# Kernel tuning notes

Hardware: AMD Instinct MI355X
Metric: run time of the kernel (lower is better)

The kernel has to match this reference:

```python
import math
import jax, jax.numpy as jnp
import numpy as np

HIDDEN = 1024

def setup_inputs() -> dict:
    key = jax.random.key(0)
    kx, kq, kk, kv = jax.random.split(key, 4)
    scale = 1.0 / math.sqrt(HIDDEN)
    x = jax.random.normal(kx, (4, 2048, HIDDEN), dtype=jnp.float32)
    # nn.Linear weights, stored as [out, in] like torch; y = x @ W.T
    Wq = jax.random.normal(kq, (HIDDEN, HIDDEN), dtype=jnp.float32) * scale
    Wk = jax.random.normal(kk, (HIDDEN, HIDDEN), dtype=jnp.float32) * scale
    Wv = jax.random.normal(kv, (HIDDEN, HIDDEN), dtype=jnp.float32) * scale
    return {"x": x, "Wq": Wq, "Wk": Wk, "Wv": Wv}

def reference(x, Wq, Wk, Wv):
    # Q,K,V: [b, s, d]
    Q = jnp.einsum('bsd,ed->bse', x, Wq)
    K = jnp.einsum('bsd,ed->bse', x, Wk)
    V = jnp.einsum('bsd,ed->bse', x, Wv)
    scores = jnp.einsum('bqd,bkd->bqk', Q, K) / math.sqrt(x.shape[-1])
    att = jax.nn.softmax(scores, axis=-1)  # stable max-subtracted softmax, same math as _softmax
    return jnp.einsum('bqk,bkd->bqd', att, V)
```

## Files before the change

### kernel.cpp

```cpp
#include <hip/hip_runtime.h>
#include <stdint.h>

typedef unsigned int uint;
typedef unsigned short ushort;
typedef __attribute__((ext_vector_type(8))) short short8;
typedef __attribute__((ext_vector_type(16))) float floatx16;

#define MEG (1024u * 1024u)

__device__ inline ushort f2b(float f) {
  union { float f; uint u; } c; c.f = f;
  uint u = c.u;
  u = (u + 0x7fffu + ((u >> 16) & 1u)) >> 16;
  return (ushort)u;
}
__device__ inline float b2f(ushort u) {
  union { uint i; float f; } c; c.i = ((uint)u) << 16; return c.f;
}

__device__ inline void gl_lds16(const ushort* g, ushort* l) {
  __builtin_amdgcn_global_load_lds(
      (const __attribute__((address_space(1))) void*)g,
      (__attribute__((address_space(3))) void*)l, 16, 0, 0);
}

__global__ __launch_bounds__(256) void cvt_all(
    const float* __restrict__ x,  const float* __restrict__ wq,
    const float* __restrict__ wk, const float* __restrict__ wv,
    ushort* __restrict__ xb, ushort* __restrict__ wb,
    float* __restrict__ ls)
{
  const int b = blockIdx.x;
  if (b >= 5632) {
    float4 z = make_float4(0.f, 0.f, 0.f, 0.f);
#pragma unroll
    for (int j = 0; j < 8; ++j)
      ((float4*)ls)[threadIdx.x * 8 + j] = z;
    return;
  }
  const float* s; ushort* d; int i;
  if (b < 4096) {
    s = x; d = xb; i = b * 256 + threadIdx.x;
  } else {
    int t = b - 4096;
    int wsel = t >> 9;
    s = (wsel == 0) ? wq : (wsel == 1) ? wk : wv;
    d = wb + (size_t)wsel * MEG;
    i = (t & 511) * 256 + threadIdx.x;
  }
  float4 a = ((const float4*)s)[i * 2];
  float4 c = ((const float4*)s)[i * 2 + 1];
  short8 v;
  v[0] = (short)f2b(a.x); v[1] = (short)f2b(a.y);
  v[2] = (short)f2b(a.z); v[3] = (short)f2b(a.w);
  v[4] = (short)f2b(c.x); v[5] = (short)f2b(c.y);
  v[6] = (short)f2b(c.z); v[7] = (short)f2b(c.w);
  ((short8*)d)[i] = v;
}

template <int MODE, int BN>
__device__ __forceinline__ void gemm_core(
    const ushort* __restrict__ A, int lda, size_t sA,
    const ushort* __restrict__ B, int ldb, size_t sB,
    void* __restrict__ C, int ldc, size_t sC,
    int K, float scale, float* __restrict__ Lsum)
{
  constexpr int NJ = BN / 64;
  constexpr int NB = BN / 32;
  __shared__ ushort As[128 * 64];
  __shared__ ushort Bs[BN * 64];

  const int tid = threadIdx.x;
  const int bz  = blockIdx.z;
  A += (size_t)bz * sA;
  B += (size_t)bz * sB;

  const int m0 = blockIdx.y * 128;
  const int n0 = blockIdx.x * BN;

  const int lane = tid & 63;
  const int w    = tid >> 6;
  const int l32  = lane & 31;
  const int lh   = lane >> 5;
  const int mw   = w >> 1;
  const int nw   = w & 1;

  const int srow = tid >> 3;
  const ushort* agp[4];
  const ushort* bgp[NB];
#pragma unroll
  for (int c4 = 0; c4 < 4; ++c4) {
    int r   = c4 * 32 + srow;
    int col = (((tid & 7) ^ ((r ^ (r >> 3)) & 7))) * 8;
    agp[c4] = A + (size_t)(m0 + r) * lda + col;
  }
#pragma unroll
  for (int cb = 0; cb < NB; ++cb) {
    int r   = cb * 32 + srow;
    int col = (((tid & 7) ^ ((r ^ (r >> 3)) & 7))) * 8;
    bgp[cb] = B + (size_t)(n0 + r) * ldb + col;
  }

  int arow[2], aswz[2], brow[NJ], bswz[NJ];
#pragma unroll
  for (int t = 0; t < 2; ++t) {
    arow[t] = mw * 64 + t * 32 + l32;
    aswz[t] = (arow[t] ^ (arow[t] >> 3)) & 7;
  }
#pragma unroll
  for (int t = 0; t < NJ; ++t) {
    brow[t] = nw * (BN / 2) + t * 32 + l32;
    bswz[t] = (brow[t] ^ (brow[t] >> 3)) & 7;
  }

  floatx16 acc[2][NJ];
#pragma unroll
  for (int i = 0; i < 2; ++i)
#pragma unroll
    for (int j = 0; j < NJ; ++j)
#pragma unroll
      for (int r = 0; r < 16; ++r) acc[i][j][r] = 0.f;

  for (int k0 = 0; k0 < K; k0 += 64) {
    __syncthreads();
#pragma unroll
    for (int c4 = 0; c4 < 4; ++c4) {
      gl_lds16(agp[c4], &As[(c4 * 32 + w * 8) * 64]);
      agp[c4] += 64;
    }
#pragma unroll
    for (int cb = 0; cb < NB; ++cb) {
      gl_lds16(bgp[cb], &Bs[(cb * 32 + w * 8) * 64]);
      bgp[cb] += 64;
    }
    __syncthreads();

#pragma unroll
    for (int s = 0; s < 4; ++s) {
      short8 af[2], bf[NJ];
#pragma unroll
      for (int t = 0; t < 2; ++t)
        af[t] = *(const short8*)&As[arow[t] * 64 + (((s * 2 + lh) ^ aswz[t]) * 8)];
#pragma unroll
      for (int t = 0; t < NJ; ++t)
        bf[t] = *(const short8*)&Bs[brow[t] * 64 + (((s * 2 + lh) ^ bswz[t]) * 8)];
#pragma unroll
      for (int i = 0; i < 2; ++i)
#pragma unroll
        for (int j = 0; j < NJ; ++j)
          acc[i][j] = __builtin_amdgcn_mfma_f32_32x32x16_bf16(
              af[i], bf[j], acc[i][j], 0, 0, 0);
    }
  }

  if constexpr (MODE == 0) {
#pragma unroll
    for (int i = 0; i < 2; ++i)
#pragma unroll
      for (int j = 0; j < NJ; ++j) {
        const int mbase = m0 + mw * 64 + i * 32 + 4 * lh;
        const int ng    = n0 + nw * (BN / 2) + j * 32 + l32;
        if (ng < 2048) {
          ushort* dst = (ushort*)C + (size_t)(ng >> 10) * (8u * MEG);
          const int nn = ng & 1023;
#pragma unroll
          for (int g = 0; g < 4; ++g)
#pragma unroll
            for (int r = 0; r < 4; ++r)
              dst[(size_t)(mbase + 8 * g + r) * 1024 + nn] =
                  f2b(acc[i][j][4 * g + r]);
        } else {
          ushort* Vo = (ushort*)C + (size_t)16 * MEG;
#pragma unroll
          for (int g = 0; g < 4; ++g) {
            uint lo = (uint)f2b(acc[i][j][4 * g + 0]) |
                      ((uint)f2b(acc[i][j][4 * g + 1]) << 16);
            uint hi = (uint)f2b(acc[i][j][4 * g + 2]) |
                      ((uint)f2b(acc[i][j][4 * g + 3]) << 16);
            *(uint2*)&Vo[(size_t)(ng - 2048) * 8192 + mbase + 8 * g] =
                make_uint2(lo, hi);
          }
        }
      }
  } else if constexpr (MODE == 1) {
    ushort* Cb = (ushort*)C + (size_t)bz * sC;
    float* Lb = Lsum + (size_t)bz * 2048;
    const int ng0 = n0 + nw * (BN / 2) + l32;
#pragma unroll
    for (int i = 0; i < 2; ++i) {
      const int mbase = m0 + mw * 64 + i * 32 + 4 * lh;
#pragma unroll
      for (int g = 0; g < 4; ++g)
#pragma unroll
        for (int r = 0; r < 4; ++r) {
          const int mg = mbase + 8 * g + r;
          float p0 = exp2f(acc[i][0][4 * g + r] * scale);
          float p1 = exp2f(acc[i][NJ - 1][4 * g + r] * scale);
          ushort u0 = f2b(p0), u1 = f2b(p1);
          Cb[(size_t)mg * ldc + ng0]      = u0;
          Cb[(size_t)mg * ldc + ng0 + 32] = u1;
          float ps = b2f(u0) + b2f(u1);
#pragma unroll
          for (int d = 1; d < 32; d <<= 1) ps += __shfl_xor(ps, d);
          if (l32 == 0) atomicAdd(&Lb[mg], ps);
        }
    }
  } else {
    float* Cb = (float*)C + (size_t)bz * sC;
    const float* Lb = Lsum + (size_t)bz * 2048;
#pragma unroll
    for (int i = 0; i < 2; ++i) {
      const int mbase = m0 + mw * 64 + i * 32 + 4 * lh;
#pragma unroll
      for (int g = 0; g < 4; ++g)
#pragma unroll
        for (int r = 0; r < 4; ++r) {
          const int mg = mbase + 8 * g + r;
          const float inv = 1.0f / Lb[mg];
#pragma unroll
          for (int j = 0; j < NJ; ++j) {
            const int ng = n0 + nw * (BN / 2) + j * 32 + l32;
            Cb[(size_t)mg * ldc + ng] = acc[i][j][4 * g + r] * inv;
          }
        }
    }
  }
}

__global__ __launch_bounds__(256, 3) void gemm_qkv(
    const ushort* __restrict__ A, int lda, size_t sA,
    const ushort* __restrict__ B, int ldb, size_t sB,
    void* __restrict__ C, int ldc, size_t sC, int K, float scale,
    float* __restrict__ Lsum) {
  gemm_core<0, 128>(A, lda, sA, B, ldb, sB, C, ldc, sC, K, scale, Lsum);
}
__global__ __launch_bounds__(256, 4) void gemm_s(
    const ushort* __restrict__ A, int lda, size_t sA,
    const ushort* __restrict__ B, int ldb, size_t sB,
    void* __restrict__ C, int ldc, size_t sC, int K, float scale,
    float* __restrict__ Lsum) {
  gemm_core<1, 128>(A, lda, sA, B, ldb, sB, C, ldc, sC, K, scale, Lsum);
}
__global__ __launch_bounds__(256, 3) void gemm_pv(
    const ushort* __restrict__ A, int lda, size_t sA,
    const ushort* __restrict__ B, int ldb, size_t sB,
    void* __restrict__ C, int ldc, size_t sC, int K, float scale,
    float* __restrict__ Lsum) {
  gemm_core<2, 128>(A, lda, sA, B, ldb, sB, C, ldc, sC, K, scale, Lsum);
}

extern "C" void kernel_launch(void* const* d_in, const int* in_sizes, int n_in,
                              void* d_out, int out_size, void* d_ws, size_t ws_size,
                              hipStream_t stream) {
  const float* x  = (const float*)d_in[0];
  const float* Wq = (const float*)d_in[1];
  const float* Wk = (const float*)d_in[2];
  const float* Wv = (const float*)d_in[3];
  float* outp = (float*)d_out;

  const float SCALE = 1.4426950408889634f / 32.0f;

  ushort* W0 = (ushort*)d_ws;
  ushort* Qb = W0;
  ushort* Kb = W0 + (size_t)8 * MEG;
  ushort* Vt = W0 + (size_t)16 * MEG;
  ushort* xb = W0 + (size_t)24 * MEG;
  ushort* Wb = W0 + (size_t)32 * MEG;
  ushort* Pb = W0 + (size_t)24 * MEG;

  const size_t NEED_FULL = ((size_t)40 * MEG) * 2 + 4 * 2048 * 4;
  const bool full = ws_size >= NEED_FULL;
  float* Ls = full ? (float*)(W0 + (size_t)40 * MEG)
                   : (float*)(W0 + (size_t)28 * MEG);

  cvt_all<<<5633, 256, 0, stream>>>(x, Wq, Wk, Wv, xb, Wb, Ls);

  gemm_qkv<<<dim3(24, 64, 1), 256, 0, stream>>>(
      xb, 1024, 0, Wb, 1024, 0, Qb, 1024, 0, 1024, 1.f, nullptr);

  if (full) {
    gemm_s<<<dim3(16, 16, 4), 256, 0, stream>>>(
        Qb, 1024, (size_t)2048 * 1024, Kb, 1024, (size_t)2048 * 1024,
        Pb, 2048, (size_t)2048 * 2048, 1024, SCALE, Ls);
    gemm_pv<<<dim3(8, 16, 4), 256, 0, stream>>>(
        Pb, 2048, (size_t)2048 * 2048, Vt, 8192, 2048,
        outp, 1024, (size_t)2048 * 1024, 2048, 1.f, Ls);
  } else {
    for (int b = 0; b < 4; ++b) {
      (void)hipMemsetAsync(Ls, 0, 2048 * sizeof(float), stream);
      gemm_s<<<dim3(16, 16, 1), 256, 0, stream>>>(
          Qb + (size_t)b * 2048 * 1024, 1024, 0,
          Kb + (size_t)b * 2048 * 1024, 1024, 0,
          Pb, 2048, 0, 1024, SCALE, Ls);
      gemm_pv<<<dim3(8, 16, 1), 256, 0, stream>>>(
          Pb, 2048, 0, Vt + (size_t)b * 2048, 8192, 0,
          outp + (size_t)b * 2048 * 1024, 1024, 0, 2048, 1.f, Ls);
    }
  }
}
```

Before: 249.1 us.

## Move GEMMs to 256-row tiles with 8 waves and a 4-stage async LDS pipeline

The shared bf16 GEMM core moves from 128xBN tiles with BK=64 and single-buffered loads to 256x256 (or 256x128) tiles with BK=32, run by 512-thread blocks. A four-slot LDS ring is filled with global_load_lds prefetches three tiles ahead. Explicit vmcnt/lgkmcnt waits, raw barriers and s_setprio around the MFMA bursts are meant to overlap global loads with matrix math and raise arithmetic intensity per block. The cost is a larger LDS footprint (about 128KB for BN=256, which limits blocks per CU), fewer blocks in the grid, and more complex hand-managed synchronisation.

Measured after the change: 265.7 us. 6.7% more time.

```diff
diff --git a/kernel.cpp b/kernel.cpp
--- a/kernel.cpp
+++ b/kernel.cpp
@@ -22,6 +22,19 @@
   __builtin_amdgcn_global_load_lds(
       (const __attribute__((address_space(1))) void*)g,
       (__attribute__((address_space(3))) void*)l, 16, 0, 0);
+}
+
+__device__ __forceinline__ void bar() {
+  asm volatile("" ::: "memory");
+  __builtin_amdgcn_s_barrier();
+  asm volatile("" ::: "memory");
+}
+template <int N>
+__device__ __forceinline__ void vm_wait() {
+  asm volatile("s_waitcnt vmcnt(%0)" :: "n"(N) : "memory");
+}
+__device__ __forceinline__ void lgkm0() {
+  asm volatile("s_waitcnt lgkmcnt(0)" ::: "memory");
 }
 
 __global__ __launch_bounds__(256) void cvt_all(
@@ -65,101 +78,177 @@
     void* __restrict__ C, int ldc, size_t sC,
     int K, float scale, float* __restrict__ Lsum)
 {
-  constexpr int NJ = BN / 64;
-  constexpr int NB = BN / 32;
-  __shared__ ushort As[128 * 64];
-  __shared__ ushort Bs[BN * 64];
+  static_assert(BN == 256 || BN == 128, "BN");
+  constexpr int BM = 256;
+  constexpr int BK = 32;
+  constexpr int WAVES_M = (BN == 256) ? 2 : 4;
+  constexpr int WAVES_N = 8 / WAVES_M;
+  constexpr int MI = BM / (WAVES_M * 32);
+  constexpr int NJ = BN / (WAVES_N * 32);
+  constexpr int A_ISS = BM / 128;
+  constexpr int B_ISS = BN / 128;
+  constexpr int LPT = A_ISS + B_ISS;
+
+  __shared__ ushort As[4 * BM * BK];
+  __shared__ ushort Bs[4 * BN * BK];
 
   const int tid = threadIdx.x;
   const int bz  = blockIdx.z;
   A += (size_t)bz * sA;
   B += (size_t)bz * sB;
 
-  const int m0 = blockIdx.y * 128;
+  const int m0 = blockIdx.y * BM;
   const int n0 = blockIdx.x * BN;
 
   const int lane = tid & 63;
   const int w    = tid >> 6;
   const int l32  = lane & 31;
   const int lh   = lane >> 5;
-  const int mw   = w >> 1;
-  const int nw   = w & 1;
-
-  const int srow = tid >> 3;
-  const ushort* agp[4];
-  const ushort* bgp[NB];
-#pragma unroll
-  for (int c4 = 0; c4 < 4; ++c4) {
-    int r   = c4 * 32 + srow;
-    int col = (((tid & 7) ^ ((r ^ (r >> 3)) & 7))) * 8;
-    agp[c4] = A + (size_t)(m0 + r) * lda + col;
-  }
-#pragma unroll
-  for (int cb = 0; cb < NB; ++cb) {
-    int r   = cb * 32 + srow;
-    int col = (((tid & 7) ^ ((r ^ (r >> 3)) & 7))) * 8;
-    bgp[cb] = B + (size_t)(n0 + r) * ldb + col;
-  }
-
-  int arow[2], aswz[2], brow[NJ], bswz[NJ];
-#pragma unroll
-  for (int t = 0; t < 2; ++t) {
-    arow[t] = mw * 64 + t * 32 + l32;
-    aswz[t] = (arow[t] ^ (arow[t] >> 3)) & 7;
-  }
-#pragma unroll
-  for (int t = 0; t < NJ; ++t) {
-    brow[t] = nw * (BN / 2) + t * 32 + l32;
-    bswz[t] = (brow[t] ^ (brow[t] >> 3)) & 7;
-  }
-
-  floatx16 acc[2][NJ];
-#pragma unroll
-  for (int i = 0; i < 2; ++i)
+  const int mw   = (BN == 256) ? (w >> 2) : (w >> 1);
+  const int nw   = (BN == 256) ? (w & 3) : (w & 1);
+
+  const int srow = tid >> 2;
+  const int sch  = tid & 3;
+  const ushort* agp[A_ISS];
+  const ushort* bgp[B_ISS];
+#pragma unroll
+  for (int q = 0; q < A_ISS; ++q) {
+    int r = q * 128 + srow;
+    agp[q] = A + (size_t)(m0 + r) * lda + ((sch ^ ((r ^ (r >> 3)) & 3)) * 8);
+  }
+#pragma unroll
+  for (int q = 0; q < B_ISS; ++q) {
+    int r = q * 128 + srow;
+    bgp[q] = B + (size_t)(n0 + r) * ldb + ((sch ^ ((r ^ (r >> 3)) & 3)) * 8);
+  }
+
+  int oa[MI], sa[MI], ob[NJ], sb[NJ];
+#pragma unroll
+  for (int i = 0; i < MI; ++i) {
+    int r = mw * (MI * 32) + i * 32 + l32;
+    oa[i] = r * BK; sa[i] = (r ^ (r >> 3)) & 3;
+  }
+#pragma unroll
+  for (int j = 0; j < NJ; ++j) {
+    int r = nw * (NJ * 32) + j * 32 + l32;
+    ob[j] = r * BK; sb[j] = (r ^ (r >> 3)) & 3;
+  }
+
+  floatx16 acc[MI][NJ];
+#pragma unroll
+  for (int i = 0; i < MI; ++i)
 #pragma unroll
     for (int j = 0; j < NJ; ++j)
 #pragma unroll
       for (int r = 0; r < 16; ++r) acc[i][j][r] = 0.f;
 
-  for (int k0 = 0; k0 < K; k0 += 64) {
-    __syncthreads();
-#pragma unroll
-    for (int c4 = 0; c4 < 4; ++c4) {
-      gl_lds16(agp[c4], &As[(c4 * 32 + w * 8) * 64]);
-      agp[c4] += 64;
-    }
-#pragma unroll
-    for (int cb = 0; cb < NB; ++cb) {
-      gl_lds16(bgp[cb], &Bs[(cb * 32 + w * 8) * 64]);
-      bgp[cb] += 64;
-    }
-    __syncthreads();
-
-#pragma unroll
-    for (int s = 0; s < 4; ++s) {
-      short8 af[2], bf[NJ];
-#pragma unroll
-      for (int t = 0; t < 2; ++t)
-        af[t] = *(const short8*)&As[arow[t] * 64 + (((s * 2 + lh) ^ aswz[t]) * 8)];
-#pragma unroll
-      for (int t = 0; t < NJ; ++t)
-        bf[t] = *(const short8*)&Bs[brow[t] * 64 + (((s * 2 + lh) ^ bswz[t]) * 8)];
+  const int nt = K / BK;
+
+#pragma unroll
+  for (int pt = 0; pt < 3; ++pt) {
+    ushort* Ad = &As[pt * (BM * BK)];
+    ushort* Bd = &Bs[pt * (BN * BK)];
+#pragma unroll
+    for (int q = 0; q < A_ISS; ++q) {
+      gl_lds16(agp[q], Ad + (q * 128 + w * 16) * BK); agp[q] += BK;
+    }
+#pragma unroll
+    for (int q = 0; q < B_ISS; ++q) {
+      gl_lds16(bgp[q], Bd + (q * 128 + w * 16) * BK); bgp[q] += BK;
+    }
+  }
+  vm_wait<2 * LPT>();
+  bar();
+
+  for (int t = 0; t < nt; ++t) {
+    const ushort* At = &As[(t & 3) * (BM * BK)];
+    const ushort* Bt = &Bs[(t & 3) * (BN * BK)];
+    ushort* Ad = &As[((t + 3) & 3) * (BM * BK)];
+    ushort* Bd = &Bs[((t + 3) & 3) * (BN * BK)];
+    const bool st = (t + 3 < nt);
+
+    short8 bf[NJ][2];
+#pragma unroll
+    for (int j = 0; j < NJ; ++j)
+#pragma unroll
+      for (int ks = 0; ks < 2; ++ks)
+        bf[j][ks] = *(const short8*)(Bt + ob[j] + ((((ks * 2) + lh) ^ sb[j]) << 3));
+
+    short8 af[2][2];
+#pragma unroll
+    for (int i = 0; i < 2; ++i)
+#pragma unroll
+      for (int ks = 0; ks < 2; ++ks)
+        af[i][ks] = *(const short8*)(At + oa[i] + ((((ks * 2) + lh) ^ sa[i]) << 3));
+    if (st) {
+#pragma unroll
+      for (int q = 0; q < A_ISS; ++q) {
+        gl_lds16(agp[q], Ad + (q * 128 + w * 16) * BK); agp[q] += BK;
+      }
+      if constexpr (BN == 128) {
+#pragma unroll
+        for (int q = 0; q < B_ISS; ++q) {
+          gl_lds16(bgp[q], Bd + (q * 128 + w * 16) * BK); bgp[q] += BK;
+        }
+      }
+    }
+    bar();
+    lgkm0();
+    __builtin_amdgcn_s_setprio(1);
+#pragma unroll
+    for (int i = 0; i < 2; ++i)
+#pragma unroll
+      for (int j = 0; j < NJ; ++j)
+#pragma unroll
+        for (int ks = 0; ks < 2; ++ks)
+          acc[i][j] = __builtin_amdgcn_mfma_f32_32x32x16_bf16(
+              af[i][ks], bf[j][ks], acc[i][j], 0, 0, 0);
+    __builtin_amdgcn_s_setprio(0);
+    if constexpr (BN == 128) {
+      if (t + 3 < nt)      vm_wait<2 * LPT>();
+      else if (t + 2 < nt) vm_wait<LPT>();
+      else                 vm_wait<0>();
+    }
+    bar();
+
+    if constexpr (BN == 256) {
 #pragma unroll
       for (int i = 0; i < 2; ++i)
 #pragma unroll
+        for (int ks = 0; ks < 2; ++ks)
+          af[i][ks] = *(const short8*)(At + oa[2 + i] + ((((ks * 2) + lh) ^ sa[2 + i]) << 3));
+      if (st) {
+#pragma unroll
+        for (int q = 0; q < B_ISS; ++q) {
+          gl_lds16(bgp[q], Bd + (q * 128 + w * 16) * BK); bgp[q] += BK;
+        }
+      }
+      bar();
+      lgkm0();
+      __builtin_amdgcn_s_setprio(1);
+#pragma unroll
+      for (int i = 0; i < 2; ++i)
+#pragma unroll
         for (int j = 0; j < NJ; ++j)
-          acc[i][j] = __builtin_amdgcn_mfma_f32_32x32x16_bf16(
-              af[i], bf[j], acc[i][j], 0, 0, 0);
+#pragma unroll
+          for (int ks = 0; ks < 2; ++ks)
+            acc[2 + i][j] = __builtin_amdgcn_mfma_f32_32x32x16_bf16(
+                af[i][ks], bf[j][ks], acc[2 + i][j], 0, 0, 0);
+      __builtin_amdgcn_s_setprio(0);
+      if (t + 3 < nt)      vm_wait<2 * LPT>();
+      else if (t + 2 < nt) vm_wait<LPT>();
+      else                 vm_wait<0>();
+      bar();
     }
   }
 
   if constexpr (MODE == 0) {
 #pragma unroll
-    for (int i = 0; i < 2; ++i)
+    for (int i = 0; i < MI; ++i)
 #pragma unroll
       for (int j = 0; j < NJ; ++j) {
-        const int mbase = m0 + mw * 64 + i * 32 + 4 * lh;
-        const int ng    = n0 + nw * (BN / 2) + j * 32 + l32;
+        const int mbase = m0 + mw * (MI * 32) + i * 32 + 4 * lh;
+        const int ng    = n0 + nw * (NJ * 32) + j * 32 + l32;
         if (ng < 2048) {
           ushort* dst = (ushort*)C + (size_t)(ng >> 10) * (8u * MEG);
           const int nn = ng & 1023;
@@ -185,10 +274,10 @@
   } else if constexpr (MODE == 1) {
     ushort* Cb = (ushort*)C + (size_t)bz * sC;
     float* Lb = Lsum + (size_t)bz * 2048;
-    const int ng0 = n0 + nw * (BN / 2) + l32;
-#pragma unroll
-    for (int i = 0; i < 2; ++i) {
-      const int mbase = m0 + mw * 64 + i * 32 + 4 * lh;
+    const int ng0 = n0 + nw * (NJ * 32) + l32;
+#pragma unroll
+    for (int i = 0; i < MI; ++i) {
+      const int mbase = m0 + mw * (MI * 32) + i * 32 + 4 * lh;
 #pragma unroll
       for (int g = 0; g < 4; ++g)
 #pragma unroll
@@ -209,8 +298,8 @@
     float* Cb = (float*)C + (size_t)bz * sC;
     const float* Lb = Lsum + (size_t)bz * 2048;
 #pragma unroll
-    for (int i = 0; i < 2; ++i) {
-      const int mbase = m0 + mw * 64 + i * 32 + 4 * lh;
+    for (int i = 0; i < MI; ++i) {
+      const int mbase = m0 + mw * (MI * 32) + i * 32 + 4 * lh;
 #pragma unroll
       for (int g = 0; g < 4; ++g)
 #pragma unroll
@@ -219,7 +308,7 @@
           const float inv = 1.0f / Lb[mg];
 #pragma unroll
           for (int j = 0; j < NJ; ++j) {
-            const int ng = n0 + nw * (BN / 2) + j * 32 + l32;
+            const int ng = n0 + nw * (NJ * 32) + j * 32 + l32;
             Cb[(size_t)mg * ldc + ng] = acc[i][j][4 * g + r] * inv;
           }
         }
@@ -227,21 +316,21 @@
   }
 }
 
-__global__ __launch_bounds__(256, 3) void gemm_qkv(
+__global__ __launch_bounds__(512, 2) void gemm_qkv(
     const ushort* __restrict__ A, int lda, size_t sA,
     const ushort* __restrict__ B, int ldb, size_t sB,
     void* __restrict__ C, int ldc, size_t sC, int K, float scale,
     float* __restrict__ Lsum) {
-  gemm_core<0, 128>(A, lda, sA, B, ldb, sB, C, ldc, sC, K, scale, Lsum);
-}
-__global__ __launch_bounds__(256, 4) void gemm_s(
+  gemm_core<0, 256>(A, lda, sA, B, ldb, sB, C, ldc, sC, K, scale, Lsum);
+}
+__global__ __launch_bounds__(512, 2) void gemm_s(
     const ushort* __restrict__ A, int lda, size_t sA,
     const ushort* __restrict__ B, int ldb, size_t sB,
     void* __restrict__ C, int ldc, size_t sC, int K, float scale,
     float* __restrict__ Lsum) {
-  gemm_core<1, 128>(A, lda, sA, B, ldb, sB, C, ldc, sC, K, scale, Lsum);
-}
-__global__ __launch_bounds__(256, 3) void gemm_pv(
+  gemm_core<1, 256>(A, lda, sA, B, ldb, sB, C, ldc, sC, K, scale, Lsum);
+}
+__global__ __launch_bounds__(512, 2) void gemm_pv(
     const ushort* __restrict__ A, int lda, size_t sA,
     const ushort* __restrict__ B, int ldb, size_t sB,
     void* __restrict__ C, int ldc, size_t sC, int K, float scale,
@@ -275,24 +364,24 @@
 
   cvt_all<<<5633, 256, 0, stream>>>(x, Wq, Wk, Wv, xb, Wb, Ls);
 
-  gemm_qkv<<<dim3(24, 64, 1), 256, 0, stream>>>(
+  gemm_qkv<<<dim3(12, 32, 1), 512, 0, stream>>>(
       xb, 1024, 0, Wb, 1024, 0, Qb, 1024, 0, 1024, 1.f, nullptr);
 
   if (full) {
-    gemm_s<<<dim3(16, 16, 4), 256, 0, stream>>>(
+    gemm_s<<<dim3(8, 8, 4), 512, 0, stream>>>(
         Qb, 1024, (size_t)2048 * 1024, Kb, 1024, (size_t)2048 * 1024,
         Pb, 2048, (size_t)2048 * 2048, 1024, SCALE, Ls);
-    gemm_pv<<<dim3(8, 16, 4), 256, 0, stream>>>(
+    gemm_pv<<<dim3(8, 8, 4), 512, 0, stream>>>(
         Pb, 2048, (size_t)2048 * 2048, Vt, 8192, 2048,
         outp, 1024, (size_t)2048 * 1024, 2048, 1.f, Ls);
   } else {
     for (int b = 0; b < 4; ++b) {
       (void)hipMemsetAsync(Ls, 0, 2048 * sizeof(float), stream);
-      gemm_s<<<dim3(16, 16, 1), 256, 0, stream>>>(
+      gemm_s<<<dim3(8, 8, 1), 512, 0, stream>>>(
           Qb + (size_t)b * 2048 * 1024, 1024, 0,
           Kb + (size_t)b * 2048 * 1024, 1024, 0,
           Pb, 2048, 0, 1024, SCALE, Ls);
-      gemm_pv<<<dim3(8, 16, 1), 256, 0, stream>>>(
+      gemm_pv<<<dim3(8, 8, 1), 512, 0, stream>>>(
           Pb, 2048, 0, Vt + (size_t)b * 2048, 8192, 0,
           outp + (size_t)b * 2048 * 1024, 1024, 0, 2048, 1.f, Ls);
     }
```

## Use 256-wide tiles with double-buffered LDS pipeline across all three GEMMs

Applied to the files above, without the earlier changes.

Each block now computes a 256xBN tile (BN 256 for the QKV and score GEMMs, 128 for the PV GEMM) with 512 threads and larger per-wave fragments. The LDS staging is double-buffered, so the next K-slice's global-to-LDS loads are issued while the current slice is consumed, and there is one barrier per iteration instead of two. Fragment reads are software-pipelined against the MFMAs, and s_setprio is raised around the matrix ops. The goal is more reuse per loaded byte and hiding load latency behind compute. The cost is 128KB of LDS per block, which allows only one block per CU, and far fewer blocks per grid (about one wave for the attention GEMMs), which can leave CUs idle or unbalanced.

Result: slower. 262.8 us (+5.5%).

```diff
diff --git a/kernel.cpp b/kernel.cpp
--- a/kernel.cpp
+++ b/kernel.cpp
@@ -65,101 +65,138 @@
     void* __restrict__ C, int ldc, size_t sC,
     int K, float scale, float* __restrict__ Lsum)
 {
-  constexpr int NJ = BN / 64;
-  constexpr int NB = BN / 32;
-  __shared__ ushort As[128 * 64];
-  __shared__ ushort Bs[BN * 64];
+  static_assert(BN == 256 || BN == 128, "BN");
+  constexpr int BM = 256;
+  constexpr int BK = 64;
+  constexpr int WM = (BN == 256) ? 2 : 4;
+  constexpr int MI = BM / (WM * 32);
+  constexpr int NJ = BN / ((8 / WM) * 32);
+  constexpr int AI = BM / 64;
+  constexpr int BI = BN / 64;
+  constexpr int ASLOT = BM * BK;
+  constexpr int BSLOT = BN * BK;
+
+  __shared__ __align__(16) ushort As[2 * ASLOT];
+  __shared__ __align__(16) ushort Bs[2 * BSLOT];
 
   const int tid = threadIdx.x;
   const int bz  = blockIdx.z;
   A += (size_t)bz * sA;
   B += (size_t)bz * sB;
 
-  const int m0 = blockIdx.y * 128;
+  const int m0 = blockIdx.y * BM;
   const int n0 = blockIdx.x * BN;
 
   const int lane = tid & 63;
   const int w    = tid >> 6;
   const int l32  = lane & 31;
   const int lh   = lane >> 5;
-  const int mw   = w >> 1;
-  const int nw   = w & 1;
+  const int mw   = (BN == 256) ? (w >> 2) : (w >> 1);
+  const int nw   = (BN == 256) ? (w & 3) : (w & 1);
 
   const int srow = tid >> 3;
-  const ushort* agp[4];
-  const ushort* bgp[NB];
-#pragma unroll
-  for (int c4 = 0; c4 < 4; ++c4) {
-    int r   = c4 * 32 + srow;
-    int col = (((tid & 7) ^ ((r ^ (r >> 3)) & 7))) * 8;
-    agp[c4] = A + (size_t)(m0 + r) * lda + col;
-  }
-#pragma unroll
-  for (int cb = 0; cb < NB; ++cb) {
-    int r   = cb * 32 + srow;
-    int col = (((tid & 7) ^ ((r ^ (r >> 3)) & 7))) * 8;
-    bgp[cb] = B + (size_t)(n0 + r) * ldb + col;
-  }
-
-  int arow[2], aswz[2], brow[NJ], bswz[NJ];
-#pragma unroll
-  for (int t = 0; t < 2; ++t) {
-    arow[t] = mw * 64 + t * 32 + l32;
-    aswz[t] = (arow[t] ^ (arow[t] >> 3)) & 7;
-  }
-#pragma unroll
-  for (int t = 0; t < NJ; ++t) {
-    brow[t] = nw * (BN / 2) + t * 32 + l32;
-    bswz[t] = (brow[t] ^ (brow[t] >> 3)) & 7;
-  }
-
-  floatx16 acc[2][NJ];
-#pragma unroll
-  for (int i = 0; i < 2; ++i)
+  const int sch  = tid & 7;
+  const ushort* agp[AI];
+  const ushort* bgp[BI];
+#pragma unroll
+  for (int q = 0; q < AI; ++q) {
+    int r = q * 64 + srow;
+    agp[q] = A + (size_t)(m0 + r) * lda + ((sch ^ ((r ^ (r >> 3)) & 7)) * 8);
+  }
+#pragma unroll
+  for (int q = 0; q < BI; ++q) {
+    int r = q * 64 + srow;
+    bgp[q] = B + (size_t)(n0 + r) * ldb + ((sch ^ ((r ^ (r >> 3)) & 7)) * 8);
+  }
+
+  int oa[MI], sa[MI], ob[NJ], sb[NJ];
+#pragma unroll
+  for (int i = 0; i < MI; ++i) {
+    int r = mw * (MI * 32) + i * 32 + l32;
+    oa[i] = r * BK; sa[i] = (r ^ (r >> 3)) & 7;
+  }
+#pragma unroll
+  for (int j = 0; j < NJ; ++j) {
+    int r = nw * (NJ * 32) + j * 32 + l32;
+    ob[j] = r * BK; sb[j] = (r ^ (r >> 3)) & 7;
+  }
+
+  floatx16 acc[MI][NJ];
+#pragma unroll
+  for (int i = 0; i < MI; ++i)
 #pragma unroll
     for (int j = 0; j < NJ; ++j)
 #pragma unroll
       for (int r = 0; r < 16; ++r) acc[i][j][r] = 0.f;
 
-  for (int k0 = 0; k0 < K; k0 += 64) {
+  const int nt = K / BK;
+
+#define STAGE(slot)                                                     \
+  {                                                                     \
+    ushort* Ad = &As[(slot) * ASLOT];                                   \
+    ushort* Bd = &Bs[(slot) * BSLOT];                                   \
+    _Pragma("unroll")                                                   \
+    for (int q = 0; q < AI; ++q) {                                      \
+      gl_lds16(agp[q], Ad + (q * 64 + w * 8) * BK); agp[q] += BK;       \
+    }                                                                   \
+    _Pragma("unroll")                                                   \
+    for (int q = 0; q < BI; ++q) {                                      \
+      gl_lds16(bgp[q], Bd + (q * 64 + w * 8) * BK); bgp[q] += BK;       \
+    }                                                                   \
+  }
+
+  STAGE(0);
+  __syncthreads();
+
+  for (int t = 0; t < nt; ++t) {
+    const ushort* At = &As[(t & 1) * ASLOT];
+    const ushort* Bt = &Bs[(t & 1) * BSLOT];
+    if (t + 1 < nt) STAGE((t + 1) & 1);
+
+    short8 af[2][MI], bf[2][NJ];
+
+#define RD(ks, buf)                                                         \
+    {                                                                       \
+      _Pragma("unroll")                                                     \
+      for (int i = 0; i < MI; ++i)                                          \
+        af[buf][i] = *(const short8*)&At[oa[i] + ((((ks)*2 + lh) ^ sa[i]) << 3)]; \
+      _Pragma("unroll")                                                     \
+      for (int j = 0; j < NJ; ++j)                                          \
+        bf[buf][j] = *(const short8*)&Bt[ob[j] + ((((ks)*2 + lh) ^ sb[j]) << 3)]; \
+    }
+#define MM(buf)                                                         \
+    {                                                                   \
+      __builtin_amdgcn_s_setprio(1);                                    \
+      _Pragma("unroll")                                                 \
+      for (int i = 0; i < MI; ++i)                                      \
+        _Pragma("unroll")                                               \
+        for (int j = 0; j < NJ; ++j)                                    \
+          acc[i][j] = __builtin_amdgcn_mfma_f32_32x32x16_bf16(          \
+              af[buf][i], bf[buf][j], acc[i][j], 0, 0, 0);              \
+      __builtin_amdgcn_s_setprio(0);                                    \
+    }
+
+    RD(0, 0);
+    RD(1, 1);
+    MM(0);
+    RD(2, 0);
+    MM(1);
+    RD(3, 1);
+    MM(0);
+    MM(1);
     __syncthreads();
-#pragma unroll
-    for (int c4 = 0; c4 < 4; ++c4) {
-      gl_lds16(agp[c4], &As[(c4 * 32 + w * 8) * 64]);
-      agp[c4] += 64;
-    }
-#pragma unroll
-    for (int cb = 0; cb < NB; ++cb) {
-      gl_lds16(bgp[cb], &Bs[(cb * 32 + w * 8) * 64]);
-      bgp[cb] += 64;
-    }
-    __syncthreads();
-
-#pragma unroll
-    for (int s = 0; s < 4; ++s) {
-      short8 af[2], bf[NJ];
-#pragma unroll
-      for (int t = 0; t < 2; ++t)
-        af[t] = *(const short8*)&As[arow[t] * 64 + (((s * 2 + lh) ^ aswz[t]) * 8)];
-#pragma unroll
-      for (int t = 0; t < NJ; ++t)
-        bf[t] = *(const short8*)&Bs[brow[t] * 64 + (((s * 2 + lh) ^ bswz[t]) * 8)];
-#pragma unroll
-      for (int i = 0; i < 2; ++i)
-#pragma unroll
-        for (int j = 0; j < NJ; ++j)
-          acc[i][j] = __builtin_amdgcn_mfma_f32_32x32x16_bf16(
-              af[i], bf[j], acc[i][j], 0, 0, 0);
-    }
-  }
+#undef RD
+#undef MM
+  }
+#undef STAGE
 
   if constexpr (MODE == 0) {
 #pragma unroll
-    for (int i = 0; i < 2; ++i)
+    for (int i = 0; i < MI; ++i)
 #pragma unroll
       for (int j = 0; j < NJ; ++j) {
-        const int mbase = m0 + mw * 64 + i * 32 + 4 * lh;
-        const int ng    = n0 + nw * (BN / 2) + j * 32 + l32;
+        const int mbase = m0 + mw * (MI * 32) + i * 32 + 4 * lh;
+        const int ng    = n0 + nw * (NJ * 32) + j * 32 + l32;
         if (ng < 2048) {
           ushort* dst = (ushort*)C + (size_t)(ng >> 10) * (8u * MEG);
           const int nn = ng & 1023;
@@ -185,10 +222,10 @@
   } else if constexpr (MODE == 1) {
     ushort* Cb = (ushort*)C + (size_t)bz * sC;
     float* Lb = Lsum + (size_t)bz * 2048;
-    const int ng0 = n0 + nw * (BN / 2) + l32;
-#pragma unroll
-    for (int i = 0; i < 2; ++i) {
-      const int mbase = m0 + mw * 64 + i * 32 + 4 * lh;
+    const int ng0 = n0 + nw * (NJ * 32) + l32;
+#pragma unroll
+    for (int i = 0; i < MI; ++i) {
+      const int mbase = m0 + mw * (MI * 32) + i * 32 + 4 * lh;
 #pragma unroll
       for (int g = 0; g < 4; ++g)
 #pragma unroll
@@ -209,8 +246,8 @@
     float* Cb = (float*)C + (size_t)bz * sC;
     const float* Lb = Lsum + (size_t)bz * 2048;
 #pragma unroll
-    for (int i = 0; i < 2; ++i) {
-      const int mbase = m0 + mw * 64 + i * 32 + 4 * lh;
+    for (int i = 0; i < MI; ++i) {
+      const int mbase = m0 + mw * (MI * 32) + i * 32 + 4 * lh;
 #pragma unroll
       for (int g = 0; g < 4; ++g)
 #pragma unroll
@@ -219,7 +256,7 @@
           const float inv = 1.0f / Lb[mg];
 #pragma unroll
           for (int j = 0; j < NJ; ++j) {
-            const int ng = n0 + nw * (BN / 2) + j * 32 + l32;
+            const int ng = n0 + nw * (NJ * 32) + j * 32 + l32;
             Cb[(size_t)mg * ldc + ng] = acc[i][j][4 * g + r] * inv;
           }
         }
@@ -227,21 +264,21 @@
   }
 }
 
-__global__ __launch_bounds__(256, 3) void gemm_qkv(
+__global__ __launch_bounds__(512, 2) void gemm_qkv(
     const ushort* __restrict__ A, int lda, size_t sA,
     const ushort* __restrict__ B, int ldb, size_t sB,
     void* __restrict__ C, int ldc, size_t sC, int K, float scale,
     float* __restrict__ Lsum) {
-  gemm_core<0, 128>(A, lda, sA, B, ldb, sB, C, ldc, sC, K, scale, Lsum);
-}
-__global__ __launch_bounds__(256, 4) void gemm_s(
+  gemm_core<0, 256>(A, lda, sA, B, ldb, sB, C, ldc, sC, K, scale, Lsum);
+}
+__global__ __launch_bounds__(512, 2) void gemm_s(
     const ushort* __restrict__ A, int lda, size_t sA,
     const ushort* __restrict__ B, int ldb, size_t sB,
     void* __restrict__ C, int ldc, size_t sC, int K, float scale,
     float* __restrict__ Lsum) {
-  gemm_core<1, 128>(A, lda, sA, B, ldb, sB, C, ldc, sC, K, scale, Lsum);
-}
-__global__ __launch_bounds__(256, 3) void gemm_pv(
+  gemm_core<1, 256>(A, lda, sA, B, ldb, sB, C, ldc, sC, K, scale, Lsum);
+}
+__global__ __launch_bounds__(512, 2) void gemm_pv(
     const ushort* __restrict__ A, int lda, size_t sA,
     const ushort* __restrict__ B, int ldb, size_t sB,
     void* __restrict__ C, int ldc, size_t sC, int K, float scale,
@@ -275,24 +312,24 @@
 
   cvt_all<<<5633, 256, 0, stream>>>(x, Wq, Wk, Wv, xb, Wb, Ls);
 
-  gemm_qkv<<<dim3(24, 64, 1), 256, 0, stream>>>(
+  gemm_qkv<<<dim3(12, 32, 1), 512, 0, stream>>>(
       xb, 1024, 0, Wb, 1024, 0, Qb, 1024, 0, 1024, 1.f, nullptr);
 
   if (full) {
-    gemm_s<<<dim3(16, 16, 4), 256, 0, stream>>>(
+    gemm_s<<<dim3(8, 8, 4), 512, 0, stream>>>(
         Qb, 1024, (size_t)2048 * 1024, Kb, 1024, (size_t)2048 * 1024,
         Pb, 2048, (size_t)2048 * 2048, 1024, SCALE, Ls);
-    gemm_pv<<<dim3(8, 16, 4), 256, 0, stream>>>(
+    gemm_pv<<<dim3(8, 8, 4), 512, 0, stream>>>(
         Pb, 2048, (size_t)2048 * 2048, Vt, 8192, 2048,
         outp, 1024, (size_t)2048 * 1024, 2048, 1.f, Ls);
   } else {
     for (int b = 0; b < 4; ++b) {
       (void)hipMemsetAsync(Ls, 0, 2048 * sizeof(float), stream);
-      gemm_s<<<dim3(16, 16, 1), 256, 0, stream>>>(
+      gemm_s<<<dim3(8, 8, 1), 512, 0, stream>>>(
           Qb + (size_t)b * 2048 * 1024, 1024, 0,
           Kb + (size_t)b * 2048 * 1024, 1024, 0,
           Pb, 2048, 0, 1024, SCALE, Ls);
-      gemm_pv<<<dim3(8, 16, 1), 256, 0, stream>>>(
+      gemm_pv<<<dim3(8, 8, 1), 512, 0, stream>>>(
           Pb, 2048, 0, Vt + (size_t)b * 2048, 8192, 0,
           outp + (size_t)b * 2048 * 1024, 1024, 0, 2048, 1.f, Ls);
     }
```

## Replace atomic row-sum accumulation with per-column-block partial sums reduced in PV GEMM

Applied to the files above, without the earlier changes.

The score GEMM now writes each warp-half's row-sum partial to its own slot instead of atomically adding into a shared row-sum buffer. The PV GEMM reduces the 32 partials for its 128 rows into shared memory at startup and reads the reciprocal from there. This removes the atomics and the zeroing pass in the conversion kernel, at the cost of a larger workspace and extra reads at the start of the PV kernel. The launch bounds for the QKV and PV GEMMs also rise to 4 blocks per CU, which may force register spilling.

Measured after the change: 245.7 us, median of 2. About the same (-1.4%).

```diff
diff --git a/kernel.cpp b/kernel.cpp
--- a/kernel.cpp
+++ b/kernel.cpp
@@ -27,17 +27,9 @@
 __global__ __launch_bounds__(256) void cvt_all(
     const float* __restrict__ x,  const float* __restrict__ wq,
     const float* __restrict__ wk, const float* __restrict__ wv,
-    ushort* __restrict__ xb, ushort* __restrict__ wb,
-    float* __restrict__ ls)
+    ushort* __restrict__ xb, ushort* __restrict__ wb)
 {
   const int b = blockIdx.x;
-  if (b >= 5632) {
-    float4 z = make_float4(0.f, 0.f, 0.f, 0.f);
-#pragma unroll
-    for (int j = 0; j < 8; ++j)
-      ((float4*)ls)[threadIdx.x * 8 + j] = z;
-    return;
-  }
   const float* s; ushort* d; int i;
   if (b < 4096) {
     s = x; d = xb; i = b * 256 + threadIdx.x;
@@ -69,6 +61,7 @@
   constexpr int NB = BN / 32;
   __shared__ ushort As[128 * 64];
   __shared__ ushort Bs[BN * 64];
+  __shared__ float Linv[(MODE == 2) ? 128 : 1];
 
   const int tid = threadIdx.x;
   const int bz  = blockIdx.z;
@@ -84,6 +77,16 @@
   const int lh   = lane >> 5;
   const int mw   = w >> 1;
   const int nw   = w & 1;
+
+  if constexpr (MODE == 2) {
+    if (tid < 128) {
+      float s = 0.f;
+#pragma unroll
+      for (int p = 0; p < 32; ++p)
+        s += Lsum[((size_t)p * gridDim.z + bz) * 2048 + m0 + tid];
+      Linv[tid] = 1.0f / s;
+    }
+  }
 
   const int srow = tid >> 3;
   const ushort* agp[4];
@@ -184,7 +187,7 @@
       }
   } else if constexpr (MODE == 1) {
     ushort* Cb = (ushort*)C + (size_t)bz * sC;
-    float* Lb = Lsum + (size_t)bz * 2048;
+    float* Lp = Lsum + ((size_t)(blockIdx.x * 2 + nw) * gridDim.z + bz) * 2048;
     const int ng0 = n0 + nw * (BN / 2) + l32;
 #pragma unroll
     for (int i = 0; i < 2; ++i) {
@@ -202,12 +205,11 @@
           float ps = b2f(u0) + b2f(u1);
 #pragma unroll
           for (int d = 1; d < 32; d <<= 1) ps += __shfl_xor(ps, d);
-          if (l32 == 0) atomicAdd(&Lb[mg], ps);
+          if (l32 == 0) Lp[mg] = ps;
         }
     }
   } else {
     float* Cb = (float*)C + (size_t)bz * sC;
-    const float* Lb = Lsum + (size_t)bz * 2048;
 #pragma unroll
     for (int i = 0; i < 2; ++i) {
       const int mbase = m0 + mw * 64 + i * 32 + 4 * lh;
@@ -216,7 +218,7 @@
 #pragma unroll
         for (int r = 0; r < 4; ++r) {
           const int mg = mbase + 8 * g + r;
-          const float inv = 1.0f / Lb[mg];
+          const float inv = Linv[mg - m0];
 #pragma unroll
           for (int j = 0; j < NJ; ++j) {
             const int ng = n0 + nw * (BN / 2) + j * 32 + l32;
@@ -227,7 +229,7 @@
   }
 }
 
-__global__ __launch_bounds__(256, 3) void gemm_qkv(
+__global__ __launch_bounds__(256, 4) void gemm_qkv(
     const ushort* __restrict__ A, int lda, size_t sA,
     const ushort* __restrict__ B, int ldb, size_t sB,
     void* __restrict__ C, int ldc, size_t sC, int K, float scale,
@@ -241,7 +243,7 @@
     float* __restrict__ Lsum) {
   gemm_core<1, 128>(A, lda, sA, B, ldb, sB, C, ldc, sC, K, scale, Lsum);
 }
-__global__ __launch_bounds__(256, 3) void gemm_pv(
+__global__ __launch_bounds__(256, 4) void gemm_pv(
     const ushort* __restrict__ A, int lda, size_t sA,
     const ushort* __restrict__ B, int ldb, size_t sB,
     void* __restrict__ C, int ldc, size_t sC, int K, float scale,
@@ -268,12 +270,12 @@
   ushort* Wb = W0 + (size_t)32 * MEG;
   ushort* Pb = W0 + (size_t)24 * MEG;
 
-  const size_t NEED_FULL = ((size_t)40 * MEG) * 2 + 4 * 2048 * 4;
+  const size_t NEED_FULL = ((size_t)40 * MEG) * 2 + (size_t)32 * 4 * 2048 * 4;
   const bool full = ws_size >= NEED_FULL;
-  float* Ls = full ? (float*)(W0 + (size_t)40 * MEG)
+  float* Lp = full ? (float*)(W0 + (size_t)40 * MEG)
                    : (float*)(W0 + (size_t)28 * MEG);
 
-  cvt_all<<<5633, 256, 0, stream>>>(x, Wq, Wk, Wv, xb, Wb, Ls);
+  cvt_all<<<5632, 256, 0, stream>>>(x, Wq, Wk, Wv, xb, Wb);
 
   gemm_qkv<<<dim3(24, 64, 1), 256, 0, stream>>>(
       xb, 1024, 0, Wb, 1024, 0, Qb, 1024, 0, 1024, 1.f, nullptr);
@@ -281,20 +283,19 @@
   if (full) {
     gemm_s<<<dim3(16, 16, 4), 256, 0, stream>>>(
         Qb, 1024, (size_t)2048 * 1024, Kb, 1024, (size_t)2048 * 1024,
-        Pb, 2048, (size_t)2048 * 2048, 1024, SCALE, Ls);
+        Pb, 2048, (size_t)2048 * 2048, 1024, SCALE, Lp);
     gemm_pv<<<dim3(8, 16, 4), 256, 0, stream>>>(
         Pb, 2048, (size_t)2048 * 2048, Vt, 8192, 2048,
-        outp, 1024, (size_t)2048 * 1024, 2048, 1.f, Ls);
+        outp, 1024, (size_t)2048 * 1024, 2048, 1.f, Lp);
   } else {
     for (int b = 0; b < 4; ++b) {
-      (void)hipMemsetAsync(Ls, 0, 2048 * sizeof(float), stream);
       gemm_s<<<dim3(16, 16, 1), 256, 0, stream>>>(
           Qb + (size_t)b * 2048 * 1024, 1024, 0,
           Kb + (size_t)b * 2048 * 1024, 1024, 0,
-          Pb, 2048, 0, 1024, SCALE, Ls);
+          Pb, 2048, 0, 1024, SCALE, Lp);
       gemm_pv<<<dim3(8, 16, 1), 256, 0, stream>>>(
           Pb, 2048, 0, Vt + (size_t)b * 2048, 8192, 0,
-          outp + (size_t)b * 2048 * 1024, 1024, 0, 2048, 1.f, Ls);
-    }
-  }
-}
+          outp + (size_t)b * 2048 * 1024, 1024, 0, 2048, 1.f, Lp);
+    }
+  }
+}
```
